# Kernel optimization log

Measured on AMD Instinct MI355X. Metric: run time of the kernel, lower is better.

Reference implementation:

```python
import jax, jax.numpy as jnp
import numpy as np
from jax import lax

B, C_IN = 8192, 1

def _conv(x, w, b):
    # x: [N,C,H,W], w: [O,I,kh,kw] valid conv, stride 1
    y = lax.conv_general_dilated(x, w, window_strides=(1, 1), padding='VALID',
                                 dimension_numbers=('NCHW', 'OIHW', 'NCHW'))
    return y + b[None, :, None, None]

def _maxpool2(x):
    return lax.reduce_window(x, -jnp.inf, lax.max, (1, 1, 2, 2), (1, 1, 2, 2), 'VALID')

def setup_inputs() -> dict:
    key = jax.random.key(0)
    ks = jax.random.split(key, 9)
    def kaiming(k, shape, fan_in):
        return jax.random.normal(k, shape, jnp.float32) * np.float32(1.0 / np.sqrt(fan_in))
    x = jax.random.normal(ks[0], (B, C_IN, 28, 28), jnp.float32)
    w1 = kaiming(ks[1], (10, C_IN, 5, 5), C_IN * 25)
    b1 = kaiming(ks[2], (10,), C_IN * 25)
    w2 = kaiming(ks[3], (20, 10, 5, 5), 10 * 25)
    b2 = kaiming(ks[4], (20,), 10 * 25)
    wl1 = kaiming(ks[5], (50, 320), 320)
    bl1 = kaiming(ks[6], (50,), 320)
    wl2 = kaiming(ks[7], (10, 50), 50)
    bl2 = kaiming(ks[8], (10,), 50)
    return {"x": x, "w1": w1, "b1": b1, "w2": w2, "b2": b2,
            "wl1": wl1, "bl1": bl1, "wl2": wl2, "bl2": bl2}

def reference(x, w1, b1, w2, b2, wl1, bl1, wl2, bl2):
    h = jax.nn.relu(_conv(x, w1, b1))       # [B,10,24,24]
    h = _maxpool2(h)                         # [B,10,12,12]
    h = jax.nn.relu(_conv(h, w2, b2))        # [B,20,8,8]
    h = _maxpool2(h)                         # [B,20,4,4]
    h = h.reshape(h.shape[0], -1)            # [B,320]
    h = jax.nn.relu(h @ wl1.T + bl1)         # [B,50]
    return h @ wl2.T + bl2                   # [B,10]
```

## Files before the change

kernel.cpp:

```cpp
#include <hip/hip_runtime.h>

#define THREADS 256
#define IPB 4

typedef _Float16 f16;
typedef _Float16 f16x2 __attribute__((ext_vector_type(2)));
typedef _Float16 f16x8 __attribute__((ext_vector_type(8)));
typedef float f32x4 __attribute__((ext_vector_type(4)));
typedef float f32x16 __attribute__((ext_vector_type(16)));
typedef unsigned int uint;

__device__ __forceinline__ f16x2 pkrtz(float a, float b) {
    return __builtin_bit_cast(f16x2, __builtin_amdgcn_cvt_pkrtz(a, b));
}
template<int CTRL>
__device__ __forceinline__ float dppmax(float v) {
    const int i = __builtin_bit_cast(int, v);
    const int s = __builtin_amdgcn_update_dpp(i, i, CTRL, 0xF, 0xF, true);
    return fmaxf(v, __builtin_bit_cast(float, s));
}

#define P1_ROW 400
#define P1_IMG 4784

__global__ void pack_weights(const float* __restrict__ w1,
                             const float* __restrict__ w2,
                             const float* __restrict__ wl1,
                             unsigned char* __restrict__ ws) {
    uint* w1pk  = (uint*)ws;
    f16x8* w2af = (f16x8*)(ws + 1024);
    f16x8* wl1pk = (f16x8*)(ws + 17408);
    const int gid = blockIdx.x * blockDim.x + threadIdx.x;
    const int gsz = gridDim.x * blockDim.x;
    for (int i = gid; i < 250; i += gsz) {
        const unsigned short u =
            __builtin_bit_cast(unsigned short, (f16)w1[i]);
        w1pk[i] = (uint)u | ((uint)u << 16);
    }
    for (int e = gid; e < 1000; e += gsz) {
        const int s = e / 40, r = e - s * 40;
        const int oc = r >> 1, h = r & 1;
        f16x8 a;
        #pragma unroll
        for (int j = 0; j < 8; ++j) {
            const int ic = h * 8 + j;
            a[j] = (f16)(ic < 10 ? w2[(oc * 10 + ic) * 25 + s] : 0.f);
        }
        w2af[e] = a;
    }
    for (int e = gid; e < 2560; e += gsz) {
        const int tile = e / 640, rem = e % 640;
        const int s = rem / 64, lane = rem % 64;
        const int m = lane & 15, quad = lane >> 4;
        const int hh = tile * 16 + m;
        f16x8 a;
        #pragma unroll
        for (int j = 0; j < 8; ++j)
            a[j] = (f16)(hh < 50 ? wl1[hh * 320 + s * 32 + quad * 8 + j] : 0.f);
        wl1pk[e] = a;
    }
}

__global__ __launch_bounds__(THREADS, 6)
void lenet_one(const float* __restrict__ x,
               const unsigned char* __restrict__ ws, const float* __restrict__ b1,
               const float* __restrict__ b2,
               const float* __restrict__ bl1,
               const float* __restrict__ wl2, const float* __restrict__ bl2,
               float* __restrict__ out, int batch)
{
    __shared__ __align__(16) unsigned char p1c[IPB * P1_IMG];
    __shared__ __align__(16) f16 p2h[IPB * 328];
    __shared__ float h1[IPB * 52];

    const uint*  w1pk  = (const uint*)ws;
    const f16x8* w2af  = (const f16x8*)(ws + 1024);
    const f16x8* wl1pk = (const f16x8*)(ws + 17408);

    const int tid = threadIdx.x;
    const int lane = tid & 63;
    const int wv_ = tid >> 6;
    const int cM = lane & 31, hK = lane >> 5;
    const int img = tid & 3;
    const int imgg = min(blockIdx.x * IPB + img, batch - 1);

    {
        const int grp = tid >> 2;
        const float* xim = x + (size_t)imgg * 784;
        for (int pq = grp; pq < 144; pq += 64) {
            const int py = pq / 12, px = pq % 12;
            const float* xb = xim + (2 * py) * 28 + 2 * px;
            float win[36];
            #pragma unroll
            for (int r = 0; r < 6; ++r)
                #pragma unroll
                for (int cc = 0; cc < 6; ++cc)
                    win[r * 6 + cc] = xb[r * 28 + cc];
            f16x2 pr[30];
            #pragma unroll
            for (int r = 0; r < 6; ++r)
                #pragma unroll
                for (int cc = 0; cc < 5; ++cc)
                    pr[r * 5 + cc] = pkrtz(win[r * 6 + cc], win[r * 6 + cc + 1]);
            f16 ch[10];
            #pragma unroll
            for (int c = 0; c < 10; ++c) {
                f16x2 accT = {(f16)0.f, (f16)0.f};
                f16x2 accB = {(f16)0.f, (f16)0.f};
                #pragma unroll
                for (int ky = 0; ky < 5; ++ky)
                    #pragma unroll
                    for (int kx = 0; kx < 5; ++kx) {
                        const uint wp = w1pk[c * 25 + ky * 5 + kx];
                        const f16x2 wv = __builtin_bit_cast(f16x2, wp);
                        accT += pr[ky * 5 + kx] * wv;
                        accB += pr[(ky + 1) * 5 + kx] * wv;
                    }
                const float q0 = fmaxf((float)accT[0], (float)accB[0]);
                const float q1 = fmaxf((float)accT[1], (float)accB[1]);
                ch[c] = (f16)fmaxf(fmaxf(q0, q1) + b1[c], 0.f);
            }
            f16x8 v0, v1;
            #pragma unroll
            for (int j = 0; j < 8; ++j) v0[j] = ch[j];
            v1[0] = ch[8]; v1[1] = ch[9];
            #pragma unroll
            for (int j = 2; j < 8; ++j) v1[j] = (f16)0.f;
            unsigned char* dst = p1c + img * P1_IMG + py * P1_ROW + px * 32;
            *(f16x8*)(dst)      = v0;
            *(f16x8*)(dst + 16) = v1;
        }
    }
    __syncthreads();

    {
        const int cy = cM >> 3, cx = cM & 7;
        const int afoff = (cM < 20 ? cM : 19) * 2 + hK;
        int bb[2];
        #pragma unroll
        for (int q = 0; q < 2; ++q) {
            const int t = wv_ * 2 + q, im = t >> 1, h2 = t & 1;
            bb[q] = im * P1_IMG + (4 * h2 + cy) * P1_ROW + cx * 32 + hK * 16;
        }
        f32x16 acc[2];
        #pragma unroll
        for (int q = 0; q < 2; ++q)
            #pragma unroll
            for (int r = 0; r < 16; ++r) acc[q][r] = 0.f;
        #pragma unroll 1
        for (int ky = 0; ky < 5; ++ky) {
            #pragma unroll
            for (int kx = 0; kx < 5; ++kx) {
                const f16x8 a = w2af[(ky * 5 + kx) * 40 + afoff];
                #pragma unroll
                for (int q = 0; q < 2; ++q) {
                    const f16x8 b =
                        *(const f16x8*)(p1c + bb[q] + ky * P1_ROW + kx * 32);
                    acc[q] = __builtin_amdgcn_mfma_f32_32x32x16_f16(a, b, acc[q],
                                                                    0, 0, 0);
                }
            }
        }
        #pragma unroll
        for (int q = 0; q < 2; ++q) {
            const int t = wv_ * 2 + q, im = t >> 1, h2 = t & 1;
            #pragma unroll
            for (int r = 0; r < 16; ++r) {
                const int m = (r & 3) + 8 * (r >> 2) + 4 * hK;
                float v = acc[q][r];
                v = dppmax<0xB1>(v);
                v = dppmax<0x128>(v);
                if (m < 20 && (lane & 9) == 0) {
                    const int py = 2 * h2 + (cM >> 4), px = cx >> 1;
                    p2h[im * 328 + m * 16 + py * 4 + px] =
                        (f16)fmaxf(v + b2[m], 0.f);
                }
            }
        }
    }
    __syncthreads();

    {
        const int n = lane & 15, quad = lane >> 4;
        f32x4 facc = {0.f, 0.f, 0.f, 0.f};
        #pragma unroll 1
        for (int s = 0; s < 10; ++s) {
            const f16x8 a = wl1pk[(wv_ * 10 + s) * 64 + lane];
            f16x8 b = {};
            if (n < IPB)
                b = *(const f16x8*)(p2h + n * 328 + s * 32 + quad * 8);
            facc = __builtin_amdgcn_mfma_f32_16x16x32_f16(a, b, facc, 0, 0, 0);
        }
        if (n < IPB) {
            #pragma unroll
            for (int r = 0; r < 4; ++r) {
                const int h = wv_ * 16 + quad * 4 + r;
                if (h < 50)
                    h1[n * 52 + h] = fmaxf(facc[r] + bl1[h], 0.f);
            }
        }
    }
    __syncthreads();

    if (tid < IPB * 10) {
        const int im = tid / 10, o = tid % 10;
        const int imgo = min(blockIdx.x * IPB + im, batch - 1);
        float a = bl2[o];
        #pragma unroll
        for (int h = 0; h < 50; ++h)
            a += h1[im * 52 + h] * wl2[o * 50 + h];
        out[(size_t)imgo * 10 + o] = a;
    }
}

extern "C" void kernel_launch(void* const* d_in, const int* in_sizes, int n_in,
                              void* d_out, int out_size, void* d_ws, size_t ws_size,
                              hipStream_t stream) {
    const float* x   = (const float*)d_in[0];
    const float* w1  = (const float*)d_in[1];
    const float* b1  = (const float*)d_in[2];
    const float* w2  = (const float*)d_in[3];
    const float* b2  = (const float*)d_in[4];
    const float* wl1 = (const float*)d_in[5];
    const float* bl1 = (const float*)d_in[6];
    const float* wl2 = (const float*)d_in[7];
    const float* bl2 = (const float*)d_in[8];
    float* out = (float*)d_out;
    unsigned char* ws = (unsigned char*)d_ws;

    const int batch = in_sizes[0] / 784;
    pack_weights<<<16, 256, 0, stream>>>(w1, w2, wl1, ws);
    const int grid = (batch + IPB - 1) / IPB;
    lenet_one<<<grid, THREADS, 0, stream>>>(x, ws, b1, b2, bl1, wl2, bl2,
                                            out, batch);
}
```

Baseline: 138.2 us.

## Stage packed fp16 input pairs in shared memory before conv1

Input images are first loaded cooperatively, with coalesced reads, into a shared-memory buffer of packed fp16 adjacent-column pairs. The conv1 threads then read their 6x5 pair windows from LDS instead of doing 36 strided global loads and 30 pack conversions each. The pool-max is done as a packed half2 max. The new staging buffer overlaps p2h/h1, which raises shared-memory use, adds a barrier, and lowers the occupancy hint from 6 to 5.

```diff
diff --git a/kernel.cpp b/kernel.cpp
--- a/kernel.cpp
+++ b/kernel.cpp
@@ -22,6 +22,10 @@
 
 #define P1_ROW 400
 #define P1_IMG 4784
+#define PAIRS_OFF 19136
+#define PAIR_IMG 812
+#define PAIR_ROW 29
+#define SMEM_BYTES 32128
 
 __global__ void pack_weights(const float* __restrict__ w1,
                              const float* __restrict__ w2,
@@ -61,7 +65,7 @@
     }
 }
 
-__global__ __launch_bounds__(THREADS, 6)
+__global__ __launch_bounds__(THREADS, 5)
 void lenet_one(const float* __restrict__ x,
                const unsigned char* __restrict__ ws, const float* __restrict__ b1,
                const float* __restrict__ b2,
@@ -69,9 +73,11 @@
                const float* __restrict__ wl2, const float* __restrict__ bl2,
                float* __restrict__ out, int batch)
 {
-    __shared__ __align__(16) unsigned char p1c[IPB * P1_IMG];
-    __shared__ __align__(16) f16 p2h[IPB * 328];
-    __shared__ float h1[IPB * 52];
+    __shared__ __align__(16) unsigned char smem[SMEM_BYTES];
+    unsigned char* p1c = smem;
+    f16x2* prl = (f16x2*)(smem + PAIRS_OFF);
+    f16*   p2h = (f16*)(smem + PAIRS_OFF);
+    float* h1  = (float*)(smem + PAIRS_OFF + 2624);
 
     const uint*  w1pk  = (const uint*)ws;
     const f16x8* w2af  = (const f16x8*)(ws + 1024);
@@ -82,26 +88,32 @@
     const int wv_ = tid >> 6;
     const int cM = lane & 31, hK = lane >> 5;
     const int img = tid & 3;
-    const int imgg = min(blockIdx.x * IPB + img, batch - 1);
+
+    for (int e = tid; e < 3136; e += THREADS) {
+        const int c = e % 28, t = e / 28;
+        const int row = t % 28, im2 = t / 28;
+        const int ig = min(blockIdx.x * IPB + im2, batch - 1);
+        f16x2 pv = {(f16)0.f, (f16)0.f};
+        if (c < 27) {
+            const float* xp = x + (size_t)ig * 784 + row * 28 + c;
+            pv = pkrtz(xp[0], xp[1]);
+        }
+        prl[im2 * PAIR_IMG + row * PAIR_ROW + c] = pv;
+    }
+    __syncthreads();
 
     {
         const int grp = tid >> 2;
-        const float* xim = x + (size_t)imgg * 784;
+        const f16x2* pbase = prl + img * PAIR_IMG;
         for (int pq = grp; pq < 144; pq += 64) {
-            const int py = pq / 12, px = pq % 12;
-            const float* xb = xim + (2 * py) * 28 + 2 * px;
-            float win[36];
-            #pragma unroll
-            for (int r = 0; r < 6; ++r)
-                #pragma unroll
-                for (int cc = 0; cc < 6; ++cc)
-                    win[r * 6 + cc] = xb[r * 28 + cc];
+            const int py = pq / 12, px = pq - py * 12;
+            const f16x2* pb = pbase + (2 * py) * PAIR_ROW + 2 * px;
             f16x2 pr[30];
             #pragma unroll
             for (int r = 0; r < 6; ++r)
                 #pragma unroll
                 for (int cc = 0; cc < 5; ++cc)
-                    pr[r * 5 + cc] = pkrtz(win[r * 6 + cc], win[r * 6 + cc + 1]);
+                    pr[r * 5 + cc] = pb[r * PAIR_ROW + cc];
             f16 ch[10];
             #pragma unroll
             for (int c = 0; c < 10; ++c) {
@@ -116,9 +128,9 @@
                         accT += pr[ky * 5 + kx] * wv;
                         accB += pr[(ky + 1) * 5 + kx] * wv;
                     }
-                const float q0 = fmaxf((float)accT[0], (float)accB[0]);
-                const float q1 = fmaxf((float)accT[1], (float)accB[1]);
-                ch[c] = (f16)fmaxf(fmaxf(q0, q1) + b1[c], 0.f);
+                const f16x2 qm = __builtin_elementwise_max(accT, accB);
+                const float q = fmaxf((float)qm[0], (float)qm[1]);
+                ch[c] = (f16)fmaxf(q + b1[c], 0.f);
             }
             f16x8 v0, v1;
             #pragma unroll
```

Result: slower. 143.7 us (+3.9%).
